# Kernel optimization log

Hardware: AMD Instinct MI355X
Metric: run time of the kernel (lower is better)

The kernel has to match this reference:

```python
import jax, jax.numpy as jnp
import numpy as np

N = 50000      # nodes
E = 800000     # edges
IN = 64        # in_channels
HID = 128      # hidden_channels
HEADS = 4
D = HID // HEADS  # 32 per-head dim
G = 64         # graphs in batch


def setup_inputs() -> dict:
    key = jax.random.key(0)
    ks = jax.random.split(key, 24)
    def p(k, shape):
        return (jax.random.normal(k, shape, jnp.float32) * 0.05)
    x = jax.random.normal(ks[0], (N, IN), jnp.float32)
    edge_index = jax.random.randint(ks[1], (2, E), 0, N, dtype=jnp.int32).astype(jnp.int64)
    batch = jnp.sort(jax.random.randint(ks[2], (N,), 0, G, dtype=jnp.int32)).astype(jnp.int64)
    inp = {"x": x, "edge_index": edge_index, "batch": batch}
    # layer 1: in -> HID (heads*D), with root/skip projection
    inp["Wq1"] = p(ks[3], (IN, HID)); inp["bq1"] = p(ks[4], (HID,))
    inp["Wk1"] = p(ks[5], (IN, HID)); inp["bk1"] = p(ks[6], (HID,))
    inp["Wv1"] = p(ks[7], (IN, HID)); inp["bv1"] = p(ks[8], (HID,))
    inp["Ws1"] = p(ks[9], (IN, HID)); inp["bs1"] = p(ks[10], (HID,))
    # layer 2: HID -> HID
    inp["Wq2"] = p(ks[11], (HID, HID)); inp["bq2"] = p(ks[12], (HID,))
    inp["Wk2"] = p(ks[13], (HID, HID)); inp["bk2"] = p(ks[14], (HID,))
    inp["Wv2"] = p(ks[15], (HID, HID)); inp["bv2"] = p(ks[16], (HID,))
    inp["Ws2"] = p(ks[17], (HID, HID)); inp["bs2"] = p(ks[18], (HID,))
    # readout linear HID -> 2
    inp["Wl"] = p(ks[19], (HID, 2)); inp["bl"] = p(ks[20], (2,))
    return inp


def transformer_conv(x, src, dst, Wq, bq, Wk, bk, Wv, bv, Ws, bs):
    """PyG TransformerConv (concat=True, root_weight=True, beta=False, eval mode)."""
    n = x.shape[0]
    q = (x @ Wq + bq).reshape(n, HEADS, D)
    k = (x @ Wk + bk).reshape(n, HEADS, D)
    v = (x @ Wv + bv).reshape(n, HEADS, D)
    # per-edge attention logits: query at target (dst), key/value at source (src)
    qi, kj, vj = q[dst], k[src], v[src]           # [E, H, D]
    logits = jnp.sum(qi * kj, axis=-1) / jnp.sqrt(jnp.asarray(D, x.dtype))  # [E, H]
    # segment softmax over incoming edges of each target node
    m = jax.ops.segment_max(logits, dst, num_segments=n)   # [N, H]
    p = jnp.exp(logits - m[dst])                           # [E, H]
    s = jax.ops.segment_sum(p, dst, num_segments=n)        # [N, H]
    alpha = p / s[dst]                                     # [E, H]
    agg = jax.ops.segment_sum(alpha[..., None] * vj, dst, num_segments=n)  # [N, H, D]
    out = agg.reshape(n, HID) + (x @ Ws + bs)              # concat heads + skip
    return out


def reference(x, edge_index, batch,
              Wq1, bq1, Wk1, bk1, Wv1, bv1, Ws1, bs1,
              Wq2, bq2, Wk2, bk2, Wv2, bv2, Ws2, bs2,
              Wl, bl):
    src, dst = edge_index[0], edge_index[1]
    h = jax.nn.relu(transformer_conv(x, src, dst, Wq1, bq1, Wk1, bk1, Wv1, bv1, Ws1, bs1))
    h = jax.nn.relu(transformer_conv(h, src, dst, Wq2, bq2, Wk2, bk2, Wv2, bv2, Ws2, bs2))
    # global mean pool per graph
    counts = jax.ops.segment_sum(jnp.ones((h.shape[0],), h.dtype), batch, num_segments=G)
    pooled = jax.ops.segment_sum(h, batch, num_segments=G) / jnp.maximum(counts, 1.0)[:, None]
    return pooled @ Wl + bl  # [G, 2]
```

## Files before the change

kernel.cpp:

```cpp
#include <hip/hip_runtime.h>
#include <hip/hip_bf16.h>
#include <cstdint>
#include <cstddef>

#define N_NODES 50000
#define N_EDGES 800000
#define IN_CH 64
#define HID_CH 128
#define N_GRAPHS 64

#define NB_CNT4 ((N_EDGES + 1023) / 1024)
#define NB_GEMM ((N_NODES + 63) / 64)
#define W_ELEMS (4 * IN_CH * 128 + 4 * HID_CH * 128)
#define NB_CONV ((W_ELEMS + 255) / 256)
#define NB_BND  ((N_NODES + 1 + 255) / 256)
#define BUCKET 64

typedef short s16x8 __attribute__((ext_vector_type(8)));
typedef float f32x4 __attribute__((ext_vector_type(4)));
typedef float f32x2 __attribute__((ext_vector_type(2)));

__device__ __forceinline__ float bf2f(__hip_bfloat16 v) { return __bfloat162float(v); }
__device__ __forceinline__ float bfbits2f(unsigned hs) {
  union { unsigned u; float f; } v; v.u = hs << 16; return v.f;
}
__device__ __forceinline__ float bfhi2f(unsigned w) {
  union { unsigned u; float f; } v; v.u = w & 0xffff0000u; return v.f;
}
__device__ __forceinline__ short f2bfs(float f) {
  __hip_bfloat16 h = __float2bfloat16(f); return *(short*)&h;
}
__device__ __forceinline__ unsigned short f2bfu(float f) {
  __hip_bfloat16 h = __float2bfloat16(f); return *(unsigned short*)&h;
}
__device__ __forceinline__ int clamp_id(int v) {
  if (v < 0) v = 0;
  if (v >= N_NODES) v = N_NODES - 1;
  return v;
}

__device__ __forceinline__ unsigned char f2fp8(float v) {
  return (unsigned char)(__builtin_amdgcn_cvt_pk_fp8_f32(v, v, 0, false) & 0xff);
}
template<bool HI>
__device__ __forceinline__ f32x2 fp8pair(unsigned w) {
  return __builtin_amdgcn_cvt_pk_f32_fp8(w, HI);
}

__device__ __forceinline__ f32x2 pkfma(f32x2 a, f32x2 b, f32x2 c) {
  f32x2 d;
  asm("v_pk_fma_f32 %0, %1, %2, %3" : "=v"(d) : "v"(a), "v"(b), "v"(c));
  return d;
}
__device__ __forceinline__ f32x2 pkadd(f32x2 a, f32x2 b) {
  f32x2 d;
  asm("v_pk_add_f32 %0, %1, %2" : "=v"(d) : "v"(a), "v"(b));
  return d;
}

__device__ __forceinline__ float quad_sum(float d) {
  d += __int_as_float(__builtin_amdgcn_mov_dpp(__float_as_int(d), 0xB1, 0xf, 0xf, true));
  d += __int_as_float(__builtin_amdgcn_mov_dpp(__float_as_int(d), 0x4E, 0xf, 0xf, true));
  return d;
}

__global__ __launch_bounds__(256)
void prep(const int* __restrict__ ei, int* __restrict__ cnt,
          unsigned short* __restrict__ rank,
          const int* __restrict__ batch, int* __restrict__ gstart,
          const float* __restrict__ w1q, const float* __restrict__ w1k,
          const float* __restrict__ w1v, const float* __restrict__ w1s,
          const float* __restrict__ w2q, const float* __restrict__ w2k,
          const float* __restrict__ w2v, const float* __restrict__ w2s,
          __hip_bfloat16* d1q, __hip_bfloat16* d1k, __hip_bfloat16* d1v, __hip_bfloat16* d1s,
          __hip_bfloat16* d2q, __hip_bfloat16* d2k, __hip_bfloat16* d2v, __hip_bfloat16* d2s)
{
  int bx = blockIdx.x;
  if (bx < NB_CNT4) {
    int e0 = bx * 1024 + threadIdx.x * 4;
    if (e0 >= N_EDGES) return;
    if (e0 + 3 < N_EDGES) {
      int4 dv = *(const int4*)(ei + N_EDGES + e0);
      unsigned short r0 = (unsigned short)atomicAdd(&cnt[clamp_id(dv.x)], 1);
      unsigned short r1 = (unsigned short)atomicAdd(&cnt[clamp_id(dv.y)], 1);
      unsigned short r2 = (unsigned short)atomicAdd(&cnt[clamp_id(dv.z)], 1);
      unsigned short r3 = (unsigned short)atomicAdd(&cnt[clamp_id(dv.w)], 1);
      ushort4 rv; rv.x = r0; rv.y = r1; rv.z = r2; rv.w = r3;
      *(ushort4*)(rank + e0) = rv;
    } else {
      for (int j = 0; j < 4; ++j)
        if (e0 + j < N_EDGES)
          rank[e0 + j] = (unsigned short)atomicAdd(&cnt[clamp_id(ei[N_EDGES + e0 + j])], 1);
    }
    return;
  }
  if (bx < NB_CNT4 + NB_CONV) {
    int j = (bx - NB_CNT4) * 256 + threadIdx.x;
    if (j >= W_ELEMS) return;
    const float* S[8] = {w1q, w1k, w1v, w1s, w2q, w2k, w2v, w2s};
    __hip_bfloat16* D[8] = {d1q, d1k, d1v, d1s, d2q, d2k, d2v, d2s};
    int m, r;
    if (j < 4 * IN_CH * 128) { m = j >> 13; r = j & 8191; }
    else { int jj = j - 4 * IN_CH * 128; m = 4 + (jj >> 14); r = jj & 16383; }
    int k = r >> 7, c = r & 127;
    D[m][(((k >> 3) * 128 + c) << 3) + (k & 7)] = __float2bfloat16(S[m][r]);
    return;
  }
  int i = (bx - NB_CNT4 - NB_CONV) * 256 + threadIdx.x;
  if (i > N_NODES) return;
  int bl = (i > 0) ? min(max(batch[i - 1], 0), N_GRAPHS - 1) : -1;
  int bc = (i < N_NODES) ? min(max(batch[i], 0), N_GRAPHS - 1) : N_GRAPHS;
  for (int g = bl + 1; g <= bc; ++g) gstart[g] = i;
}

template<int KD, int XF32>
__device__ __forceinline__ void gemm_body(
    int bg, const void* X,
    const short* __restrict__ WTq, const short* __restrict__ WTk,
    const short* __restrict__ WTv, const short* __restrict__ WTs,
    const float* __restrict__ bq, const float* __restrict__ bk,
    const float* __restrict__ bv, const float* __restrict__ bs,
    short* Qo, unsigned char* KV8, short* So, short* lds)
{
  constexpr int KT = KD / 32;
  constexpr int CHUNKS = KD * 16;
  const int tid  = threadIdx.x;
  const int wid  = tid >> 6;
  const int lane = tid & 63;
  const int quad = lane >> 4;
  const int mm   = lane & 15;
  const int rt   = wid & 1;
  const int ch   = wid >> 1;
  const int rowbase = bg * 64 + rt * 32;

  s16x8 afrag[2][KT];
  #pragma unroll
  for (int t = 0; t < 2; ++t) {
    const int arow = rowbase + t * 16 + mm;
    if (arow < N_NODES) {
      if (XF32) {
        const float* xp = (const float*)X + (size_t)arow * KD;
        #pragma unroll
        for (int kt = 0; kt < KT; ++kt) {
          const float4* p = (const float4*)(xp + kt * 32 + quad * 8);
          float4 a = p[0], b = p[1];
          s16x8 fr;
          fr[0] = f2bfs(a.x); fr[1] = f2bfs(a.y); fr[2] = f2bfs(a.z); fr[3] = f2bfs(a.w);
          fr[4] = f2bfs(b.x); fr[5] = f2bfs(b.y); fr[6] = f2bfs(b.z); fr[7] = f2bfs(b.w);
          afrag[t][kt] = fr;
        }
      } else {
        const short* xp = (const short*)X + (size_t)arow * KD;
        #pragma unroll
        for (int kt = 0; kt < KT; ++kt)
          afrag[t][kt] = *(const s16x8*)(xp + kt * 32 + quad * 8);
      }
    } else {
      #pragma unroll
      for (int kt = 0; kt < KT; ++kt)
        afrag[t][kt] = (s16x8){0,0,0,0,0,0,0,0};
    }
  }

  const short* wts[4] = {WTq, WTk, WTv, WTs};
  const float* bias[4] = {bq, bk, bv, bs};

  #pragma unroll
  for (int mat = 0; mat < 4; ++mat) {
    if (mat > 0) __syncthreads();
    {
      const uint4* src = (const uint4*)wts[mat];
      uint4* dst = (uint4*)lds;
      #pragma unroll
      for (int i = 0; i < CHUNKS / 256; ++i)
        dst[tid + i * 256] = src[tid + i * 256];
    }
    __syncthreads();

    f32x4 acc[4][2];
    #pragma unroll
    for (int c4 = 0; c4 < 4; ++c4) {
      float b = bias[mat][ch * 64 + c4 * 16 + mm];
      f32x4 av = {b, b, b, b};
      acc[c4][0] = av; acc[c4][1] = av;
    }
    #pragma unroll
    for (int kt = 0; kt < KT; ++kt) {
      #pragma unroll
      for (int c4 = 0; c4 < 4; ++c4) {
        s16x8 bfrag = *(const s16x8*)(lds + ((((kt * 4 + quad) << 7) + ch * 64 + c4 * 16 + mm) << 3));
        acc[c4][0] = __builtin_amdgcn_mfma_f32_16x16x32_bf16(afrag[0][kt], bfrag, acc[c4][0], 0, 0, 0);
        acc[c4][1] = __builtin_amdgcn_mfma_f32_16x16x32_bf16(afrag[1][kt], bfrag, acc[c4][1], 0, 0, 0);
      }
    }
    if (mat == 1 || mat == 2) {
      const int voff = (mat == 2) ? 8 : 0;
      #pragma unroll
      for (int c4 = 0; c4 < 4; ++c4) {
        const int col = ch * 64 + c4 * 16 + mm;
        const int bpos = ((col >> 3) << 4) + voff + (col & 7);
        #pragma unroll
        for (int t = 0; t < 2; ++t) {
          #pragma unroll
          for (int r = 0; r < 4; ++r) {
            int row = rowbase + t * 16 + quad * 4 + r;
            if (row < N_NODES)
              KV8[(size_t)row * 256 + bpos] = f2fp8(acc[c4][t][r]);
          }
        }
      }
    } else {
      short* O = (mat == 0) ? Qo : So;
      #pragma unroll
      for (int c4 = 0; c4 < 4; ++c4) {
        const int col = ch * 64 + c4 * 16 + mm;
        #pragma unroll
        for (int t = 0; t < 2; ++t) {
          #pragma unroll
          for (int r = 0; r < 4; ++r) {
            int row = rowbase + t * 16 + quad * 4 + r;
            if (row < N_NODES)
              ((__hip_bfloat16*)O)[(size_t)row * 128 + col] = __float2bfloat16(acc[c4][t][r]);
          }
        }
      }
    }
  }
}

__global__ __launch_bounds__(256)
void scatter_gemm1(const int* __restrict__ ei, const unsigned short* __restrict__ rank,
                   int* __restrict__ ssrc,
                   const float* __restrict__ X,
                   const short* __restrict__ w1q, const short* __restrict__ w1k,
                   const short* __restrict__ w1v, const short* __restrict__ w1s,
                   const float* __restrict__ b1q, const float* __restrict__ b1k,
                   const float* __restrict__ b1v, const float* __restrict__ b1s,
                   short* Qb, unsigned char* KV8, short* Sb)
{
  __shared__ short lds[IN_CH * 128];
  int bx = blockIdx.x;
  if (bx >= NB_GEMM) {
    int e0 = (bx - NB_GEMM) * 1024 + threadIdx.x * 4;
    if (e0 >= N_EDGES) return;
    if (e0 + 3 < N_EDGES) {
      int4 sv = *(const int4*)(ei + e0);
      int4 dv = *(const int4*)(ei + N_EDGES + e0);
      ushort4 rv = *(const ushort4*)(rank + e0);
      if (rv.x < BUCKET) ssrc[(clamp_id(dv.x) << 6) + rv.x] = clamp_id(sv.x);
      if (rv.y < BUCKET) ssrc[(clamp_id(dv.y) << 6) + rv.y] = clamp_id(sv.y);
      if (rv.z < BUCKET) ssrc[(clamp_id(dv.z) << 6) + rv.z] = clamp_id(sv.z);
      if (rv.w < BUCKET) ssrc[(clamp_id(dv.w) << 6) + rv.w] = clamp_id(sv.w);
    } else {
      for (int j = 0; j < 4; ++j) {
        int e = e0 + j;
        if (e < N_EDGES) {
          unsigned short r = rank[e];
          if (r < BUCKET)
            ssrc[(clamp_id(ei[N_EDGES + e]) << 6) + r] = clamp_id(ei[e]);
        }
      }
    }
    return;
  }
  gemm_body<IN_CH, 1>(bx, X, w1q, w1k, w1v, w1s, b1q, b1k, b1v, b1s,
                      Qb, KV8, Sb, lds);
}

__global__ __launch_bounds__(256)
void attn_kernel(const unsigned short* __restrict__ Q, const unsigned char* __restrict__ KV8,
                 const unsigned short* S, const int* __restrict__ cnt,
                 const int* __restrict__ ssrc, unsigned short* H)
{
  const int dst = blockIdx.x * 4 + (threadIdx.x >> 6);
  if (dst >= N_NODES) return;
  const int lane = threadIdx.x & 63;
  const int sub  = lane >> 4;
  const int cl   = lane & 15;

  const float qs = 0.17677669529663687f * 1.4426950408889634f;
  uint4 qw = *(const uint4*)(Q + (size_t)dst * 128 + cl * 8);
  uint4 sw = *(const uint4*)(S + (size_t)dst * 128 + cl * 8);
  f32x2 q2[4], a2[4];
  #pragma unroll
  for (int i = 0; i < 4; ++i) {
    unsigned w = ((unsigned*)&qw)[i];
    f32x2 t; t.x = bfbits2f(w & 0xffffu) * qs; t.y = bfhi2f(w) * qs;
    q2[i] = t;
    a2[i].x = 0.f; a2[i].y = 0.f;
  }
  float s = 0.f;

  const int deg = min(cnt[dst], BUCKET);
  const int e0 = dst << 6;
  const int iters = (deg + 3) >> 2;

  int allsrc = (lane < deg) ? ssrc[e0 + lane] : 0;

  if (iters > 0) {
    auto kvload = [&](int it) -> uint4 {
      int sidx = __shfl(allsrc, 4 * it + sub, 64);
      return *(const uint4*)(KV8 + (size_t)sidx * 256 + cl * 16);
    };
    uint4 kva = kvload(0);
    uint4 kvb = kvload(1);

    for (int it = 0; it < iters; ++it) {
      uint4 kv = kva;
      kva = kvb;
      if (it + 2 < iters) kvb = kvload(it + 2);
      const float ph = (4 * it + sub < deg) ? 1.f : 0.f;
      f32x2 k0 = fp8pair<false>(kv.x), k1 = fp8pair<true>(kv.x);
      f32x2 k2 = fp8pair<false>(kv.y), k3 = fp8pair<true>(kv.y);
      f32x2 zz; zz.x = 0.f; zz.y = 0.f;
      f32x2 dd = pkfma(q2[0], k0, zz);
      dd = pkfma(q2[1], k1, dd);
      dd = pkfma(q2[2], k2, dd);
      dd = pkfma(q2[3], k3, dd);
      float d = quad_sum(dd.x + dd.y);
      float p = exp2f(d) * ph;
      s += p;
      f32x2 p2; p2.x = p; p2.y = p;
      f32x2 v0 = fp8pair<false>(kv.z), v1 = fp8pair<true>(kv.z);
      f32x2 v2 = fp8pair<false>(kv.w), v3 = fp8pair<true>(kv.w);
      a2[0] = pkfma(p2, v0, a2[0]);
      a2[1] = pkfma(p2, v1, a2[1]);
      a2[2] = pkfma(p2, v2, a2[2]);
      a2[3] = pkfma(p2, v3, a2[3]);
    }
  }

  s += __shfl_xor(s, 16, 64);
  s += __shfl_xor(s, 32, 64);
  #pragma unroll
  for (int i = 0; i < 4; ++i) {
    f32x2 t;
    t.x = __shfl_xor(a2[i].x, 16, 64);
    t.y = __shfl_xor(a2[i].y, 16, 64);
    a2[i] = pkadd(a2[i], t);
    t.x = __shfl_xor(a2[i].x, 32, 64);
    t.y = __shfl_xor(a2[i].y, 32, 64);
    a2[i] = pkadd(a2[i], t);
  }
  const float inv = (s > 0.f) ? (1.0f / s) : 0.f;

  if (sub == 0) {
    uint4 ow;
    #pragma unroll
    for (int i = 0; i < 4; ++i) {
      unsigned w = ((unsigned*)&sw)[i];
      float o0 = fmaxf(a2[i].x * inv + bfbits2f(w & 0xffffu), 0.f);
      float o1 = fmaxf(a2[i].y * inv + bfhi2f(w), 0.f);
      ((unsigned*)&ow)[i] = (unsigned)f2bfu(o0) | ((unsigned)f2bfu(o1) << 16);
    }
    *(uint4*)(H + (size_t)dst * 128 + cl * 8) = ow;
  }
}

__global__ __launch_bounds__(256)
void gemm2(const short* __restrict__ X,
           const short* __restrict__ w2q, const short* __restrict__ w2k,
           const short* __restrict__ w2v, const short* __restrict__ w2s,
           const float* __restrict__ b2q, const float* __restrict__ b2k,
           const float* __restrict__ b2v, const float* __restrict__ b2s,
           short* Qb, unsigned char* KV8, short* Sb)
{
  __shared__ short lds[HID_CH * 128];
  gemm_body<HID_CH, 0>(blockIdx.x, X, w2q, w2k, w2v, w2s, b2q, b2k, b2v, b2s,
                       Qb, KV8, Sb, lds);
}

__global__ __launch_bounds__(128)
void pool_partial(const __hip_bfloat16* __restrict__ H, const int* __restrict__ gstart,
                  float* __restrict__ pooled)
{
  const int g = blockIdx.x >> 4, p = blockIdx.x & 15, t = threadIdx.x;
  const int s = gstart[g];
  const int e = gstart[g + 1];
  const int len = e - s;
  if (len <= 0) return;
  const int chunk = (len + 15) >> 4;
  const int a = s + p * chunk;
  const int b = min(a + chunk, e);
  if (a >= b) return;
  float s0 = 0.f, s1 = 0.f, s2 = 0.f, s3 = 0.f;
  int i = a;
  for (; i + 3 < b; i += 4) {
    s0 += bf2f(H[(size_t)i * 128 + t]);
    s1 += bf2f(H[(size_t)(i + 1) * 128 + t]);
    s2 += bf2f(H[(size_t)(i + 2) * 128 + t]);
    s3 += bf2f(H[(size_t)(i + 3) * 128 + t]);
  }
  for (; i < b; ++i) s0 += bf2f(H[(size_t)i * 128 + t]);
  atomicAdd(&pooled[g * 128 + t], (s0 + s1) + (s2 + s3));
}

__global__ __launch_bounds__(128)
void pool_final(const float* __restrict__ pooled, const int* __restrict__ gstart,
                const float* __restrict__ Wl, const float* __restrict__ bl,
                float* __restrict__ out)
{
  const int g = blockIdx.x, t = threadIdx.x;
  __shared__ float r0[128], r1[128];
  const int len = gstart[g + 1] - gstart[g];
  const float inv = 1.0f / (float)max(len, 1);
  const float pc = pooled[g * 128 + t] * inv;
  r0[t] = pc * Wl[t * 2 + 0];
  r1[t] = pc * Wl[t * 2 + 1];
  __syncthreads();
  for (int o = 64; o > 0; o >>= 1) {
    if (t < o) { r0[t] += r0[t + o]; r1[t] += r1[t + o]; }
    __syncthreads();
  }
  if (t == 0) {
    out[g * 2 + 0] = r0[0] + bl[0];
    out[g * 2 + 1] = r1[0] + bl[1];
  }
}


extern "C" void kernel_launch(void* const* d_in, const int* in_sizes, int n_in,
                              void* d_out, int out_size, void* d_ws, size_t ws_size,
                              hipStream_t stream) {
  uintptr_t base = (uintptr_t)d_ws;
  auto take = [&](size_t bytes) -> uintptr_t {
    uintptr_t p = base;
    base += (bytes + 255) & ~(size_t)255;
    return p;
  };

  int*   cnt    = (int*)take((size_t)N_NODES * 4);
  float* pooled = (float*)take((size_t)N_GRAPHS * 128 * 4);
  int*   gstart = (int*)take((size_t)(N_GRAPHS + 1) * 4);
  int*   ssrc   = (int*)take((size_t)N_NODES * BUCKET * 4);
  unsigned short* rank = (unsigned short*)take((size_t)N_EDGES * 2);
  short* Qb     = (short*)take((size_t)N_NODES * 128 * 2);
  unsigned char* KV8 = (unsigned char*)take((size_t)N_NODES * 256);
  short* Sb     = (short*)take((size_t)N_NODES * 128 * 2);
  short* wt1q   = (short*)take((size_t)IN_CH * 128 * 2);
  short* wt1k   = (short*)take((size_t)IN_CH * 128 * 2);
  short* wt1v   = (short*)take((size_t)IN_CH * 128 * 2);
  short* wt1s   = (short*)take((size_t)IN_CH * 128 * 2);
  short* wt2q   = (short*)take((size_t)HID_CH * 128 * 2);
  short* wt2k   = (short*)take((size_t)HID_CH * 128 * 2);
  short* wt2v   = (short*)take((size_t)HID_CH * 128 * 2);
  short* wt2s   = (short*)take((size_t)HID_CH * 128 * 2);

  const int* ei    = (const int*)d_in[1];
  const int* batch = (const int*)d_in[2];

  size_t zspan = (size_t)((char*)gstart + (size_t)(N_GRAPHS + 1) * 4 - (char*)cnt);
  hipMemsetAsync(cnt, 0, zspan, stream);

  prep<<<NB_CNT4 + NB_CONV + NB_BND, 256, 0, stream>>>(
      ei, cnt, rank, batch, gstart,
      (const float*)d_in[3], (const float*)d_in[5], (const float*)d_in[7], (const float*)d_in[9],
      (const float*)d_in[11], (const float*)d_in[13], (const float*)d_in[15], (const float*)d_in[17],
      (__hip_bfloat16*)wt1q, (__hip_bfloat16*)wt1k, (__hip_bfloat16*)wt1v, (__hip_bfloat16*)wt1s,
      (__hip_bfloat16*)wt2q, (__hip_bfloat16*)wt2k, (__hip_bfloat16*)wt2v, (__hip_bfloat16*)wt2s);

  scatter_gemm1<<<NB_GEMM + NB_CNT4, 256, 0, stream>>>(
      ei, rank, ssrc,
      (const float*)d_in[0],
      wt1q, wt1k, wt1v, wt1s,
      (const float*)d_in[4], (const float*)d_in[6], (const float*)d_in[8], (const float*)d_in[10],
      Qb, KV8, Sb);

  const int attn_grid = (N_NODES + 3) / 4;

  attn_kernel<<<attn_grid, 256, 0, stream>>>(
      (const unsigned short*)Qb, KV8,
      (const unsigned short*)Sb, cnt, ssrc, (unsigned short*)Sb);

  gemm2<<<NB_GEMM, 256, 0, stream>>>(
      Sb, wt2q, wt2k, wt2v, wt2s,
      (const float*)d_in[12], (const float*)d_in[14], (const float*)d_in[16], (const float*)d_in[18],
      Qb, KV8, Sb);

  attn_kernel<<<attn_grid, 256, 0, stream>>>(
      (const unsigned short*)Qb, KV8,
      (const unsigned short*)Sb, cnt, ssrc, (unsigned short*)Sb);

  pool_partial<<<N_GRAPHS * 16, 128, 0, stream>>>(
      (const __hip_bfloat16*)Sb, gstart, pooled);
  pool_final<<<N_GRAPHS, 128, 0, stream>>>(pooled, gstart, (const float*)d_in[19],
                                           (const float*)d_in[20], (float*)d_out);
}
```

Measured before the change: 262.8 us.

## Double-buffer GEMM weight tiles in LDS using direct global-to-LDS loads

Replaces the serial copy-then-compute weight staging in the shared GEMM body with a two-buffer pipeline. Each weight matrix is split into 64-row halves, and the next half is loaded into the other LDS buffer with global_load_lds while MFMAs run on the current one. The goal is to hide weight-load latency and drop the register round-trip of the old copy. The cost is extra synchronisation steps, a fixed 32 KB LDS allocation, and dependence on the compiler emitting the right waits for the async LDS loads.

```diff
diff --git a/kernel.cpp b/kernel.cpp
--- a/kernel.cpp
+++ b/kernel.cpp
@@ -62,6 +62,12 @@
   d += __int_as_float(__builtin_amdgcn_mov_dpp(__float_as_int(d), 0xB1, 0xf, 0xf, true));
   d += __int_as_float(__builtin_amdgcn_mov_dpp(__float_as_int(d), 0x4E, 0xf, 0xf, true));
   return d;
+}
+
+__device__ __forceinline__ void gload_lds16(const void* g, void* l) {
+  __builtin_amdgcn_global_load_lds(
+      (const __attribute__((address_space(1))) unsigned int*)g,
+      (__attribute__((address_space(3))) unsigned int*)l, 16, 0, 0);
 }
 
 __global__ __launch_bounds__(256)
@@ -120,10 +126,11 @@
     const short* __restrict__ WTv, const short* __restrict__ WTs,
     const float* __restrict__ bq, const float* __restrict__ bk,
     const float* __restrict__ bv, const float* __restrict__ bs,
-    short* Qo, unsigned char* KV8, short* So, short* lds)
+    short* Qo, unsigned char* KV8, short* So, short* lds )
 {
   constexpr int KT = KD / 32;
-  constexpr int CHUNKS = KD * 16;
+  constexpr int HALVES = KD / 64;
+  constexpr int STEPS = 4 * HALVES;
   const int tid  = threadIdx.x;
   const int wid  = tid >> 6;
   const int lane = tid & 63;
@@ -132,6 +139,20 @@
   const int rt   = wid & 1;
   const int ch   = wid >> 1;
   const int rowbase = bg * 64 + rt * 32;
+
+  const short* wts[4] = {WTq, WTk, WTv, WTs};
+  const float* bias[4] = {bq, bk, bv, bs};
+
+  auto stage = [&](int s) {
+    const short* src = wts[s / HALVES] + (s % HALVES) * 8192;
+    short* dstb = lds + (s & 1) * 8192;
+    #pragma unroll
+    for (int i = 0; i < 4; ++i)
+      gload_lds16(src + (size_t)(i * 256 + tid) * 8,
+                  dstb + (size_t)(i * 256 + wid * 64) * 8);
+  };
+
+  stage(0);
 
   s16x8 afrag[2][KT];
   #pragma unroll
@@ -162,69 +183,70 @@
     }
   }
 
-  const short* wts[4] = {WTq, WTk, WTv, WTs};
-  const float* bias[4] = {bq, bk, bv, bs};
-
+  __syncthreads();
+
+  f32x4 acc[4][2];
   #pragma unroll
-  for (int mat = 0; mat < 4; ++mat) {
-    if (mat > 0) __syncthreads();
-    {
-      const uint4* src = (const uint4*)wts[mat];
-      uint4* dst = (uint4*)lds;
-      #pragma unroll
-      for (int i = 0; i < CHUNKS / 256; ++i)
-        dst[tid + i * 256] = src[tid + i * 256];
-    }
-    __syncthreads();
-
-    f32x4 acc[4][2];
-    #pragma unroll
-    for (int c4 = 0; c4 < 4; ++c4) {
-      float b = bias[mat][ch * 64 + c4 * 16 + mm];
-      f32x4 av = {b, b, b, b};
-      acc[c4][0] = av; acc[c4][1] = av;
-    }
-    #pragma unroll
-    for (int kt = 0; kt < KT; ++kt) {
+  for (int s = 0; s < STEPS; ++s) {
+    const int mat  = s / HALVES;
+    const int half = s % HALVES;
+    const short* bufp = lds + (s & 1) * 8192;
+
+    if (half == 0) {
       #pragma unroll
       for (int c4 = 0; c4 < 4; ++c4) {
-        s16x8 bfrag = *(const s16x8*)(lds + ((((kt * 4 + quad) << 7) + ch * 64 + c4 * 16 + mm) << 3));
-        acc[c4][0] = __builtin_amdgcn_mfma_f32_16x16x32_bf16(afrag[0][kt], bfrag, acc[c4][0], 0, 0, 0);
-        acc[c4][1] = __builtin_amdgcn_mfma_f32_16x16x32_bf16(afrag[1][kt], bfrag, acc[c4][1], 0, 0, 0);
+        float b = bias[mat][ch * 64 + c4 * 16 + mm];
+        f32x4 av = {b, b, b, b};
+        acc[c4][0] = av; acc[c4][1] = av;
       }
     }
-    if (mat == 1 || mat == 2) {
-      const int voff = (mat == 2) ? 8 : 0;
+    if (s + 1 < STEPS) stage(s + 1);
+
+    #pragma unroll
+    for (int ktl = 0; ktl < 2; ++ktl) {
       #pragma unroll
       for (int c4 = 0; c4 < 4; ++c4) {
-        const int col = ch * 64 + c4 * 16 + mm;
-        const int bpos = ((col >> 3) << 4) + voff + (col & 7);
+        s16x8 bfrag = *(const s16x8*)(bufp + ((((ktl * 4 + quad) << 7) + ch * 64 + c4 * 16 + mm) << 3));
+        acc[c4][0] = __builtin_amdgcn_mfma_f32_16x16x32_bf16(afrag[0][half * 2 + ktl], bfrag, acc[c4][0], 0, 0, 0);
+        acc[c4][1] = __builtin_amdgcn_mfma_f32_16x16x32_bf16(afrag[1][half * 2 + ktl], bfrag, acc[c4][1], 0, 0, 0);
+      }
+    }
+
+    if (half == HALVES - 1) {
+      if (mat == 1 || mat == 2) {
+        const int voff = (mat == 2) ? 8 : 0;
         #pragma unroll
-        for (int t = 0; t < 2; ++t) {
+        for (int c4 = 0; c4 < 4; ++c4) {
+          const int col = ch * 64 + c4 * 16 + mm;
+          const int bpos = ((col >> 3) << 4) + voff + (col & 7);
           #pragma unroll
-          for (int r = 0; r < 4; ++r) {
-            int row = rowbase + t * 16 + quad * 4 + r;
-            if (row < N_NODES)
-              KV8[(size_t)row * 256 + bpos] = f2fp8(acc[c4][t][r]);
+          for (int t = 0; t < 2; ++t) {
+            #pragma unroll
+            for (int r = 0; r < 4; ++r) {
+              int row = rowbase + t * 16 + quad * 4 + r;
+              if (row < N_NODES)
+                KV8[(size_t)row * 256 + bpos] = f2fp8(acc[c4][t][r]);
+            }
+          }
+        }
+      } else {
+        short* O = (mat == 0) ? Qo : So;
+        #pragma unroll
+        for (int c4 = 0; c4 < 4; ++c4) {
+          const int col = ch * 64 + c4 * 16 + mm;
+          #pragma unroll
+          for (int t = 0; t < 2; ++t) {
+            #pragma unroll
+            for (int r = 0; r < 4; ++r) {
+              int row = rowbase + t * 16 + quad * 4 + r;
+              if (row < N_NODES)
+                ((__hip_bfloat16*)O)[(size_t)row * 128 + col] = __float2bfloat16(acc[c4][t][r]);
+            }
           }
         }
       }
-    } else {
-      short* O = (mat == 0) ? Qo : So;
-      #pragma unroll
-      for (int c4 = 0; c4 < 4; ++c4) {
-        const int col = ch * 64 + c4 * 16 + mm;
-        #pragma unroll
-        for (int t = 0; t < 2; ++t) {
-          #pragma unroll
-          for (int r = 0; r < 4; ++r) {
-            int row = rowbase + t * 16 + quad * 4 + r;
-            if (row < N_NODES)
-              ((__hip_bfloat16*)O)[(size_t)row * 128 + col] = __float2bfloat16(acc[c4][t][r]);
-          }
-        }
-      }
-    }
+    }
+    if (s + 1 < STEPS) __syncthreads();
   }
 }
 
@@ -238,7 +260,7 @@
                    const float* __restrict__ b1v, const float* __restrict__ b1s,
                    short* Qb, unsigned char* KV8, short* Sb)
 {
-  __shared__ short lds[IN_CH * 128];
+  __shared__ short lds[2 * 64 * 128];
   int bx = blockIdx.x;
   if (bx >= NB_GEMM) {
     int e0 = (bx - NB_GEMM) * 1024 + threadIdx.x * 4;
@@ -365,7 +387,7 @@
            const float* __restrict__ b2v, const float* __restrict__ b2s,
            short* Qb, unsigned char* KV8, short* Sb)
 {
-  __shared__ short lds[HID_CH * 128];
+  __shared__ short lds[2 * 64 * 128];
   gemm_body<HID_CH, 0>(blockIdx.x, X, w2q, w2k, w2v, w2s, b2q, b2k, b2v, b2s,
                        Qb, KV8, Sb, lds);
 }
```

Measured after the change: 260.4 us. No clear change (-0.9%).
